# Optimization experiments

Measured on AMD Instinct MI355X. Metric: run time of the kernel, lower is better.

The kernel has to match this reference:

```python
import jax, jax.numpy as jnp
import numpy as np

NUM_GRAPHS = 128
EPS = 1e-5


def _instance_norm(x, seg, num_seg):
    # Per-graph instance norm over rows grouped by seg (PyG InstanceNorm, affine=False).
    ones = jnp.ones((x.shape[0], 1), x.dtype)
    cnt = jnp.maximum(jax.ops.segment_sum(ones, seg, num_segments=num_seg), 1.0)  # [G,1]
    mean = jax.ops.segment_sum(x, seg, num_segments=num_seg) / cnt               # [G,C]
    xc = x - mean[seg]
    var = jax.ops.segment_sum(xc * xc, seg, num_segments=num_seg) / cnt          # [G,C]
    return xc * jax.lax.rsqrt(var[seg] + EPS)


def setup_inputs() -> dict:
    key = jax.random.key(0)
    ks = jax.random.split(key, 8)
    N, E, H, G = 50000, 800000, 64, NUM_GRAPHS
    emb = jax.random.normal(ks[0], (N, H), dtype=jnp.float32)
    edge_index = jax.random.randint(ks[1], (2, E), 0, N, dtype=jnp.int64)
    batch = jnp.sort(jax.random.randint(ks[2], (N,), 0, G, dtype=jnp.int64))
    s1 = 1.0 / np.sqrt(2 * H)
    s2 = 1.0 / np.sqrt(4 * H)
    s3 = 1.0 / np.sqrt(H)
    return {
        "emb": emb,
        "edge_index": edge_index,
        "batch": batch,
        "W1": jax.random.normal(ks[3], (2 * H, 4 * H), dtype=jnp.float32) * s1,
        "b1": jnp.zeros((4 * H,), jnp.float32),
        "W2": jax.random.normal(ks[4], (4 * H, H), dtype=jnp.float32) * s2,
        "b2": jnp.zeros((H,), jnp.float32),
        "W3": jax.random.normal(ks[5], (H, 1), dtype=jnp.float32) * s3,
        "b3": jnp.zeros((1,), jnp.float32),
    }


def reference(emb, edge_index, batch, W1, b1, W2, b2, W3, b3):
    col, row = edge_index[0], edge_index[1]
    # Gather both endpoint embeddings and concat: [E, 2H]
    f12 = jnp.concatenate([emb[col], emb[row]], axis=-1)
    seg = batch[col]  # graph id per edge
    # MLP([2H, 4H, H, 1]): Linear -> InstanceNorm(batch) -> ReLU (dropout=identity in eval)
    h = jnp.maximum(_instance_norm(f12 @ W1 + b1, seg, NUM_GRAPHS), 0.0)
    h = jnp.maximum(_instance_norm(h @ W2 + b2, seg, NUM_GRAPHS), 0.0)
    att_log_logits = h @ W3 + b3  # [E, 1]
    return att_log_logits
```

## Files before the change

kernel.cpp:

```cpp
#include <hip/hip_runtime.h>
#include <hip/hip_bf16.h>
#include <stdint.h>

#define NG 128
#define EPSI 1e-5f

typedef __attribute__((ext_vector_type(8))) __bf16 bf16x8;
typedef __attribute__((ext_vector_type(4))) float f32x4;
typedef unsigned int u32x4 __attribute__((ext_vector_type(4)));

union ABFrag { bf16x8 v; unsigned short u[8]; uint4 q; };
union U8 { uint4 q; unsigned short u[8]; u32x4 e; };

__device__ __forceinline__ float b2f(unsigned short u){
  union { unsigned int i; float f; } v; v.i = ((unsigned int)u) << 16; return v.f;
}
__device__ __forceinline__ unsigned short f2b(float f){
  union { float f; unsigned int i; } v; v.f = f;
  unsigned int r = v.i + 0x7fffu + ((v.i >> 16) & 1u);
  return (unsigned short)(r >> 16);
}
__device__ __forceinline__ unsigned int pk2(float lo, float hi){
  unsigned int r;
  asm("v_cvt_pk_bf16_f32 %0, %1, %2" : "=v"(r) : "v"(lo), "v"(hi));
  return r;
}

__global__ void kprep(const float* __restrict__ emb, const float* __restrict__ W1,
                      const float* __restrict__ W2,
                      const int* __restrict__ ei,
                      unsigned short* __restrict__ embb, unsigned short* __restrict__ WcF,
                      unsigned short* __restrict__ W2F,
                      unsigned int* __restrict__ nodeh, int N, int E){
  int idx = blockIdx.x * 256 + threadIdx.x;
  int stride = gridDim.x * 256;
  int embCnt4 = N * 16;
  for (int i = idx; i < embCnt4; i += stride){
    float4 v = *(const float4*)(emb + (size_t)i * 4);
    ushort4 o; o.x = f2b(v.x); o.y = f2b(v.y); o.z = f2b(v.z); o.w = f2b(v.w);
    *(ushort4*)(embb + (size_t)i * 4) = o;
  }
  for (int i = idx; i < 32 * 2 * 64 * 8; i += stride){
    int j = i & 7, lane = (i >> 3) & 63, ks = (i >> 9) & 1, tn = i >> 10;
    int quad = lane >> 4, l15 = lane & 15;
    int k = ks * 32 + quad * 8 + j;
    int n = tn * 16 + l15;
    float wv = (n < 256) ? W1[k * 256 + n] : W1[(k + 64) * 256 + (n - 256)];
    WcF[i] = f2b(wv);
  }
  for (int i = idx; i < 4 * 8 * 64 * 8; i += stride){
    int j = i & 7, lane = (i >> 3) & 63, ks = (i >> 9) & 7, w = i >> 12;
    int quad = lane >> 4, l15 = lane & 15;
    W2F[i] = f2b(W2[(ks * 32 + quad * 8 + j) * 64 + w * 16 + l15]);
  }
  for (int e = idx; e < E; e += stride)
    atomicAdd(&nodeh[ei[e]], 1u);
}

__global__ void khist(const unsigned int* __restrict__ nodeh, const int* __restrict__ batch,
                      unsigned int* __restrict__ hist, int N){
  __shared__ unsigned int h[NG];
  for (int i = threadIdx.x; i < NG; i += 256) h[i] = 0;
  __syncthreads();
  int idx = blockIdx.x * 256 + threadIdx.x;
  for (int i = idx; i < N; i += gridDim.x * 256)
    atomicAdd(&h[batch[i]], nodeh[i]);
  __syncthreads();
  for (int i = threadIdx.x; i < NG; i += 256)
    if (h[i]) atomicAdd(&hist[i], h[i]);
}

__global__ void __launch_bounds__(256) kscan(const unsigned int* __restrict__ nodeh,
                      const unsigned int* __restrict__ hist,
                      const int* __restrict__ batch,
                      unsigned int* __restrict__ ncursor,
                      unsigned int* __restrict__ gmeta,
                      int* __restrict__ ecn, int* __restrict__ ern,
                      int* __restrict__ eorig, int* __restrict__ tilegid, int N){
  __shared__ unsigned int sh[3];
  __shared__ unsigned int wtot[4];
  int g = blockIdx.x;
  int t = threadIdx.x;
  unsigned int part = 0;
  for (int i = t; i < g; i += 256) part += (hist[i] + 31u) & ~31u;
  #pragma unroll
  for (int d = 1; d < 64; d <<= 1) part += __shfl_xor(part, d);
  if ((t & 63) == 0) wtot[t >> 6] = part;
  if (t == 64 || t == 65){
    int target = g + (t - 64);
    int lo = 0, hi = N;
    while (lo < hi){ int mid = (lo + hi) >> 1; if (batch[mid] < target) lo = mid + 1; else hi = mid; }
    sh[1 + (t - 64)] = lo;
  }
  __syncthreads();
  if (t == 0){
    unsigned int pb = wtot[0] + wtot[1] + wtot[2] + wtot[3];
    sh[0] = pb;
    gmeta[g] = pb;
    if (g == NG - 1) gmeta[NG] = pb + ((hist[g] + 31u) & ~31u);
  }
  __syncthreads();
  unsigned int run = sh[0];
  {
    unsigned int cnt = hist[g];
    unsigned int pe = (cnt + 31u) & ~31u;
    for (unsigned int i = cnt + t; i < pe; i += 256){
      ecn[run + i] = 0; ern[run + i] = 0; eorig[run + i] = -1;
    }
    unsigned int nt = pe >> 5, tb = run >> 5;
    for (unsigned int i = t; i < nt; i += 256) tilegid[tb + i] = g;
  }
  int lo = (int)sh[1], hi = (int)sh[2];
  int wid = t >> 6;
  for (int base = lo; base < hi; base += 256){
    int i = base + t;
    unsigned int v = (i < hi) ? nodeh[i] : 0u;
    unsigned int x = v;
    #pragma unroll
    for (int d = 1; d < 64; d <<= 1){
      unsigned int y = __shfl_up(x, d);
      if ((t & 63) >= d) x += y;
    }
    if ((t & 63) == 63) wtot[wid] = x;
    __syncthreads();
    unsigned int woff = 0;
    #pragma unroll
    for (int wb = 0; wb < 4; ++wb) if (wb < wid) woff += wtot[wb];
    if (i < hi) ncursor[i] = run + woff + x - v;
    run += wtot[0] + wtot[1] + wtot[2] + wtot[3];
    __syncthreads();
  }
}

__global__ void kscatter(const int* __restrict__ ei, int E,
                         unsigned int* __restrict__ ncursor,
                         int* __restrict__ ecn, int* __restrict__ ern,
                         int* __restrict__ eorig){
  int idx = blockIdx.x * 256 + threadIdx.x;
  for (int e = idx; e < E; e += gridDim.x * 256){
    int cn = ei[e], rn = ei[E + e];
    unsigned int p = atomicAdd(&ncursor[cn], 1u);
    ecn[p] = cn; ern[p] = rn; eorig[p] = e;
  }
}

__global__ void __launch_bounds__(256) kgemm1(const unsigned short* __restrict__ embb,
    const unsigned short* __restrict__ WcF, const float* __restrict__ b1,
    unsigned short* __restrict__ PQb, int Nn){
  int wave = threadIdx.x >> 6, lane = threadIdx.x & 63;
  int quad = lane >> 4, l15 = lane & 15;
  int tm = blockIdx.x * 4 + wave;
  int tmmax = (Nn + 15) >> 4;
  if (tm >= tmmax) return;
  int m = tm * 16 + l15; if (m >= Nn) m = Nn - 1;
  ABFrag a0, a1;
  a0.q = *(const uint4*)(embb + (size_t)m * 64 + quad * 8);
  a1.q = *(const uint4*)(embb + (size_t)m * 64 + 32 + quad * 8);
  int rowbase = tm * 16 + quad * 4;
  #pragma unroll 4
  for (int tn = 0; tn < 32; ++tn){
    ABFrag b0, b1f;
    b0.q  = *(const uint4*)(WcF + ((size_t)(tn * 2 + 0) * 64 + lane) * 8);
    b1f.q = *(const uint4*)(WcF + ((size_t)(tn * 2 + 1) * 64 + lane) * 8);
    f32x4 acc = {0.f, 0.f, 0.f, 0.f};
    acc = __builtin_amdgcn_mfma_f32_16x16x32_bf16(a0.v, b0.v, acc, 0, 0, 0);
    acc = __builtin_amdgcn_mfma_f32_16x16x32_bf16(a1.v, b1f.v, acc, 0, 0, 0);
    int col = tn * 16 + l15;
    float bias = (col < 256) ? b1[col] : 0.0f;
    #pragma unroll
    for (int r = 0; r < 4; ++r){
      int rowg = rowbase + r;
      if (rowg < Nn) PQb[(size_t)rowg * 512 + col] = f2b(acc[r] + bias);
    }
  }
}

__global__ void __launch_bounds__(256) kstats1(const unsigned short* __restrict__ PQb,
    const int* __restrict__ ern, const int* __restrict__ batch,
    const unsigned int* __restrict__ ncursor, const unsigned int* __restrict__ nodeh,
    float* __restrict__ sum1, float* __restrict__ sq1, int N){
  __shared__ float lsum[4][256];
  __shared__ float lsq[4][256];
  int tid = threadIdx.x;
  for (int i = tid; i < 4 * 256; i += 256){ ((float*)lsum)[i] = 0.f; ((float*)lsq)[i] = 0.f; }
  __syncthreads();
  int base = blockIdx.x * 32;
  int gfirst = batch[base];
  int wid = tid >> 6, lane = tid & 63;
  int c4 = lane * 4;
  float T1[4] = {0.f,0.f,0.f,0.f}, T2[4] = {0.f,0.f,0.f,0.f};
  int curg = -1;
  auto flushT = [&](){
    if (curg >= 0){
      unsigned slot = (unsigned)(curg - gfirst);
      if (slot < 4u){
        #pragma unroll
        for (int t = 0; t < 4; ++t){
          atomicAdd(&lsum[slot][c4 + t], T1[t]);
          atomicAdd(&lsq[slot][c4 + t], T2[t]);
        }
      } else {
        #pragma unroll
        for (int t = 0; t < 4; ++t){
          atomicAdd(&sum1[curg * 256 + c4 + t], T1[t]);
          atomicAdd(&sq1[curg * 256 + c4 + t], T2[t]);
        }
      }
      #pragma unroll
      for (int t = 0; t < 4; ++t){ T1[t] = 0.f; T2[t] = 0.f; }
    }
  };
  for (int i = 0; i < 8; ++i){
    int n = base + wid + i * 4;
    if (n >= N) break;
    int g = batch[n];
    unsigned int cnt = nodeh[n];
    if (g != curg){ flushT(); curg = g; }
    if (!cnt) continue;
    unsigned int start = ncursor[n] - cnt;
    ushort4 pv = *(const ushort4*)(PQb + (size_t)n * 512 + c4);
    float S1[4] = {0.f,0.f,0.f,0.f}, S2[4] = {0.f,0.f,0.f,0.f};
    for (unsigned int jb = 0; jb < cnt; jb += 64){
      int jn = (int)min(64u, cnt - jb);
      int rnv = (lane < jn) ? __builtin_nontemporal_load(&ern[start + jb + (unsigned)lane]) : 0;
      #pragma unroll 4
      for (int j = 0; j < jn; ++j){
        int rn = __shfl(rnv, j);
        ushort4 qv = *(const ushort4*)(PQb + (size_t)rn * 512 + 256 + c4);
        float q0 = b2f(qv.x), q1 = b2f(qv.y), q2 = b2f(qv.z), q3 = b2f(qv.w);
        S1[0] += q0; S2[0] = fmaf(q0, q0, S2[0]);
        S1[1] += q1; S2[1] = fmaf(q1, q1, S2[1]);
        S1[2] += q2; S2[2] = fmaf(q2, q2, S2[2]);
        S1[3] += q3; S2[3] = fmaf(q3, q3, S2[3]);
      }
    }
    float fc = (float)cnt;
    float p0 = b2f(pv.x), p1 = b2f(pv.y), p2 = b2f(pv.z), p3 = b2f(pv.w);
    T1[0] += fmaf(fc, p0, S1[0]);  T2[0] += fmaf(fmaf(fc, p0, 2.f * S1[0]), p0, S2[0]);
    T1[1] += fmaf(fc, p1, S1[1]);  T2[1] += fmaf(fmaf(fc, p1, 2.f * S1[1]), p1, S2[1]);
    T1[2] += fmaf(fc, p2, S1[2]);  T2[2] += fmaf(fmaf(fc, p2, 2.f * S1[2]), p2, S2[2]);
    T1[3] += fmaf(fc, p3, S1[3]);  T2[3] += fmaf(fmaf(fc, p3, 2.f * S1[3]), p3, S2[3]);
  }
  flushT();
  __syncthreads();
  for (int i = tid; i < 4 * 256; i += 256){
    int slot = i >> 8, ch = i & 255;
    float vs = lsum[slot][ch], vq = lsq[slot][ch];
    if (vs != 0.f || vq != 0.f){
      int g = gfirst + slot;
      atomicAdd(&sum1[g * 256 + ch], vs);
      atomicAdd(&sq1[g * 256 + ch], vq);
    }
  }
}

__global__ void kfin(const float* __restrict__ sum, const float* __restrict__ sq,
                     const unsigned int* __restrict__ hist,
                     float* __restrict__ meanA, float* __restrict__ rstdA, int C){
  int i = blockIdx.x * blockDim.x + threadIdx.x;
  if (i >= NG * C) return;
  int g = i / C;
  float cnt = fmaxf((float)hist[g], 1.0f);
  float m = sum[i] / cnt;
  float v = sq[i] / cnt - m * m;
  meanA[i] = m;
  rstdA[i] = rsqrtf(fmaxf(v, 0.f) + EPSI);
}

__global__ void __launch_bounds__(256) knorm1(unsigned short* __restrict__ PQb,
    const int* __restrict__ batch, const float* __restrict__ mean1,
    const float* __restrict__ rstd1, int N){
  int idx = blockIdx.x * 256 + threadIdx.x;
  if (idx >= N * 32) return;
  int n = idx >> 5, c8 = (idx & 31) * 8;
  int g = batch[n];
  unsigned short* pp = PQb + (size_t)n * 512 + c8;
  U8 pu; pu.q = *(const uint4*)pp;
  const float* mg = mean1 + g * 256 + c8;
  const float* rg = rstd1 + g * 256 + c8;
  float4 m0 = *(const float4*)mg, m1 = *(const float4*)(mg + 4);
  float4 r0 = *(const float4*)rg, r1 = *(const float4*)(rg + 4);
  U8 o;
  o.q.x = pk2((b2f(pu.u[0]) - m0.x) * r0.x, (b2f(pu.u[1]) - m0.y) * r0.y);
  o.q.y = pk2((b2f(pu.u[2]) - m0.z) * r0.z, (b2f(pu.u[3]) - m0.w) * r0.w);
  o.q.z = pk2((b2f(pu.u[4]) - m1.x) * r1.x, (b2f(pu.u[5]) - m1.y) * r1.y);
  o.q.w = pk2((b2f(pu.u[6]) - m1.z) * r1.z, (b2f(pu.u[7]) - m1.w) * r1.w);
  *(uint4*)pp = o.q;
}

__global__ void __launch_bounds__(256, 5) kmain(const unsigned short* __restrict__ PQb,
    const unsigned short* __restrict__ W2F,
    const int* __restrict__ ecn, const int* __restrict__ ern,
    const int* __restrict__ tilegid,
    const float* __restrict__ rstd1, const float* __restrict__ b2,
    const unsigned int* __restrict__ hist, const unsigned int* __restrict__ gmeta,
    unsigned short* __restrict__ y2b, float* __restrict__ sum2, float* __restrict__ sq2){
  __shared__ unsigned short Blds[4 * 8 * 64 * 8];
  {
    const uint4* src = (const uint4*)W2F;
    uint4* dst = (uint4*)Blds;
    for (int i = threadIdx.x; i < 2048; i += 256) dst[i] = src[i];
  }
  __syncthreads();
  int wave = threadIdx.x >> 6, lane = threadIdx.x & 63;
  int quad = lane >> 4, l15 = lane & 15;
  float b2v[4];
  #pragma unroll
  for (int cg = 0; cg < 4; ++cg) b2v[cg] = b2[cg * 16 + l15];
  int ntiles = (int)(gmeta[NG] >> 5);
  int nw = gridDim.x * 4;
  for (int t = blockIdx.x * 4 + wave; t < ntiles; t += nw){
    int p0 = t * 32;
    int g = __builtin_amdgcn_readfirstlane(tilegid[t]);
    int cn0 = __builtin_nontemporal_load(&ecn[p0 + l15]);
    int rn0 = __builtin_nontemporal_load(&ern[p0 + l15]);
    int cn1 = __builtin_nontemporal_load(&ecn[p0 + 16 + l15]);
    int rn1 = __builtin_nontemporal_load(&ern[p0 + 16 + l15]);
    const unsigned short* pp0 = PQb + (size_t)cn0 * 512 + quad * 8;
    const unsigned short* qq0 = PQb + (size_t)rn0 * 512 + 256 + quad * 8;
    const unsigned short* pp1 = PQb + (size_t)cn1 * 512 + quad * 8;
    const unsigned short* qq1 = PQb + (size_t)rn1 * 512 + 256 + quad * 8;
    const float* rr = rstd1 + g * 256 + quad * 8;
    f32x4 acc[8];
    #pragma unroll
    for (int i = 0; i < 8; ++i){ acc[i][0]=0.f; acc[i][1]=0.f; acc[i][2]=0.f; acc[i][3]=0.f; }
    #pragma unroll 2
    for (int ks = 0; ks < 8; ++ks){
      U8 pu0, qu0, pu1, qu1;
      pu0.q = *(const uint4*)(pp0 + ks * 32);
      qu0.q = *(const uint4*)(qq0 + ks * 32);
      pu1.q = *(const uint4*)(pp1 + ks * 32);
      qu1.q = *(const uint4*)(qq1 + ks * 32);
      float4 ra = *(const float4*)(rr + ks * 32);
      float4 rb = *(const float4*)(rr + ks * 32 + 4);
      ABFrag a0, a1;
      a0.q.x = pk2(fmaxf(0.f, b2f(pu0.u[0]) + b2f(qu0.u[0]) * ra.x),
                   fmaxf(0.f, b2f(pu0.u[1]) + b2f(qu0.u[1]) * ra.y));
      a0.q.y = pk2(fmaxf(0.f, b2f(pu0.u[2]) + b2f(qu0.u[2]) * ra.z),
                   fmaxf(0.f, b2f(pu0.u[3]) + b2f(qu0.u[3]) * ra.w));
      a0.q.z = pk2(fmaxf(0.f, b2f(pu0.u[4]) + b2f(qu0.u[4]) * rb.x),
                   fmaxf(0.f, b2f(pu0.u[5]) + b2f(qu0.u[5]) * rb.y));
      a0.q.w = pk2(fmaxf(0.f, b2f(pu0.u[6]) + b2f(qu0.u[6]) * rb.z),
                   fmaxf(0.f, b2f(pu0.u[7]) + b2f(qu0.u[7]) * rb.w));
      a1.q.x = pk2(fmaxf(0.f, b2f(pu1.u[0]) + b2f(qu1.u[0]) * ra.x),
                   fmaxf(0.f, b2f(pu1.u[1]) + b2f(qu1.u[1]) * ra.y));
      a1.q.y = pk2(fmaxf(0.f, b2f(pu1.u[2]) + b2f(qu1.u[2]) * ra.z),
                   fmaxf(0.f, b2f(pu1.u[3]) + b2f(qu1.u[3]) * ra.w));
      a1.q.z = pk2(fmaxf(0.f, b2f(pu1.u[4]) + b2f(qu1.u[4]) * rb.x),
                   fmaxf(0.f, b2f(pu1.u[5]) + b2f(qu1.u[5]) * rb.y));
      a1.q.w = pk2(fmaxf(0.f, b2f(pu1.u[6]) + b2f(qu1.u[6]) * rb.z),
                   fmaxf(0.f, b2f(pu1.u[7]) + b2f(qu1.u[7]) * rb.w));
      #pragma unroll
      for (int cg = 0; cg < 4; ++cg){
        ABFrag b;
        b.q = *(const uint4*)&Blds[((cg * 8 + ks) * 64 + lane) * 8];
        acc[cg]     = __builtin_amdgcn_mfma_f32_16x16x32_bf16(a0.v, b.v, acc[cg], 0, 0, 0);
        acc[4 + cg] = __builtin_amdgcn_mfma_f32_16x16x32_bf16(a1.v, b.v, acc[4 + cg], 0, 0, 0);
      }
    }
    #pragma unroll
    for (int sub = 0; sub < 2; ++sub)
      #pragma unroll
      for (int r = 0; r < 4; ++r){
        int el = sub * 16 + quad * 4 + r;
        size_t rowo = (size_t)(p0 + el) * 64 + l15;
        #pragma unroll
        for (int cg = 0; cg < 4; ++cg)
          y2b[rowo + cg * 16] = f2b(acc[sub * 4 + cg][r] + b2v[cg]);
      }
    int nl = (int)gmeta[g] + (int)hist[g] - p0;
    #pragma unroll
    for (int cg = 0; cg < 4; ++cg){
      float s = 0.f, qs = 0.f;
      #pragma unroll
      for (int sub = 0; sub < 2; ++sub)
        #pragma unroll
        for (int r = 0; r < 4; ++r){
          int el = sub * 16 + quad * 4 + r;
          if (el < nl){
            float y = acc[sub * 4 + cg][r] + b2v[cg];
            s += y; qs = fmaf(y, y, qs);
          }
        }
      s  += __shfl_xor(s, 16);  s  += __shfl_xor(s, 32);
      qs += __shfl_xor(qs, 16); qs += __shfl_xor(qs, 32);
      if (quad == 0){
        atomicAdd(&sum2[g * 64 + cg * 16 + l15], s);
        atomicAdd(&sq2[g * 64 + cg * 16 + l15], qs);
      }
    }
  }
}

__global__ void kfinal(const unsigned short* __restrict__ y2b,
                       const int* __restrict__ eorig, const int* __restrict__ tilegid,
                       const unsigned int* __restrict__ gmeta,
                       const float* __restrict__ mean2, const float* __restrict__ rstd2,
                       const float* __restrict__ W3, const float* __restrict__ b3,
                       float* __restrict__ out){
  int EP = (int)gmeta[NG];
  int sub = threadIdx.x & 7;
  int c8 = sub * 8;
  float w3r[8];
  #pragma unroll
  for (int t = 0; t < 8; ++t) w3r[t] = W3[c8 + t];
  float b3v = b3[0];
  int step = (gridDim.x * blockDim.x) >> 3;
  for (int i = (blockIdx.x * blockDim.x + threadIdx.x) >> 3; i < EP; i += step){
    int orig = __builtin_nontemporal_load(&eorig[i]);
    int gz = tilegid[i >> 5];
    U8 yv; yv.e = __builtin_nontemporal_load((const u32x4*)(y2b + (size_t)i * 64 + c8));
    const float* mg = mean2 + gz * 64 + c8;
    const float* rg = rstd2 + gz * 64 + c8;
    float4 m0 = *(const float4*)mg, m1 = *(const float4*)(mg + 4);
    float4 r0 = *(const float4*)rg, r1 = *(const float4*)(rg + 4);
    float a = 0.f;
    a += fmaxf(0.f, (b2f(yv.u[0]) - m0.x) * r0.x) * w3r[0];
    a += fmaxf(0.f, (b2f(yv.u[1]) - m0.y) * r0.y) * w3r[1];
    a += fmaxf(0.f, (b2f(yv.u[2]) - m0.z) * r0.z) * w3r[2];
    a += fmaxf(0.f, (b2f(yv.u[3]) - m0.w) * r0.w) * w3r[3];
    a += fmaxf(0.f, (b2f(yv.u[4]) - m1.x) * r1.x) * w3r[4];
    a += fmaxf(0.f, (b2f(yv.u[5]) - m1.y) * r1.y) * w3r[5];
    a += fmaxf(0.f, (b2f(yv.u[6]) - m1.z) * r1.z) * w3r[6];
    a += fmaxf(0.f, (b2f(yv.u[7]) - m1.w) * r1.w) * w3r[7];
    a += __shfl_xor(a, 1);
    a += __shfl_xor(a, 2);
    a += __shfl_xor(a, 4);
    if (sub == 0 && orig >= 0) out[orig] = a + b3v;
  }
}

extern "C" void kernel_launch(void* const* d_in, const int* in_sizes, int n_in,
                              void* d_out, int out_size, void* d_ws, size_t ws_size,
                              hipStream_t stream){
  const float* emb  = (const float*)d_in[0];
  const int*   ei   = (const int*)d_in[1];
  const int*   batch= (const int*)d_in[2];
  const float* W1   = (const float*)d_in[3];
  const float* b1   = (const float*)d_in[4];
  const float* W2   = (const float*)d_in[5];
  const float* b2   = (const float*)d_in[6];
  const float* W3   = (const float*)d_in[7];
  const float* b3   = (const float*)d_in[8];
  int N = in_sizes[0] / 64;
  int E = in_sizes[1] / 2;
  int EPMAX = E + NG * 32;
  float* out = (float*)d_out;

  char* w = (char*)d_ws;
  size_t off = 0;
  auto nxt = [&](size_t bytes) -> char* {
    char* p = w + off;
    off = (off + bytes + 255) & ~(size_t)255;
    return p;
  };
  unsigned short* embb = (unsigned short*)nxt((size_t)N * 64 * 2);
  unsigned short* WcF  = (unsigned short*)nxt(32 * 2 * 64 * 8 * 2);
  unsigned short* W2F  = (unsigned short*)nxt(4 * 8 * 64 * 8 * 2);
  unsigned short* PQb  = (unsigned short*)nxt((size_t)N * 512 * 2);
  unsigned short* y2b  = (unsigned short*)nxt((size_t)EPMAX * 64 * 2);
  int* ecn   = (int*)nxt((size_t)EPMAX * 4);
  int* ern   = (int*)nxt((size_t)EPMAX * 4);
  int* eorig = (int*)nxt((size_t)EPMAX * 4);
  int* tilegid = (int*)nxt((size_t)(EPMAX / 32 + 1) * 4);
  float* mean1 = (float*)nxt(NG * 256 * 4);
  float* rstd1 = (float*)nxt(NG * 256 * 4);
  float* mean2 = (float*)nxt(NG * 64 * 4);
  float* rstd2 = (float*)nxt(NG * 64 * 4);
  unsigned int* ncursor = (unsigned int*)nxt((size_t)N * 4);
  unsigned int* gmeta   = (unsigned int*)nxt((NG + 1) * 4);
  char* zbase = w + off;
  unsigned int* hist  = (unsigned int*)nxt(NG * 4);
  unsigned int* nodeh = (unsigned int*)nxt((size_t)N * 4);
  float* sum1 = (float*)nxt(NG * 256 * 4);
  float* sq1  = (float*)nxt(NG * 256 * 4);
  float* sum2 = (float*)nxt(NG * 64 * 4);
  float* sq2  = (float*)nxt(NG * 64 * 4);
  size_t zbytes = (size_t)((w + off) - zbase);
  hipMemsetAsync(zbase, 0, zbytes, stream);

  kprep<<<2048, 256, 0, stream>>>(emb, W1, W2, ei, embb, WcF, W2F, nodeh, N, E);
  khist<<<64, 256, 0, stream>>>(nodeh, batch, hist, N);
  kscan<<<NG, 256, 0, stream>>>(nodeh, hist, batch, ncursor, gmeta,
                                ecn, ern, eorig, tilegid, N);
  kscatter<<<2048, 256, 0, stream>>>(ei, E, ncursor, ecn, ern, eorig);
  {
    int tmmax = (N + 15) / 16;
    kgemm1<<<(tmmax + 3) / 4, 256, 0, stream>>>(embb, WcF, b1, PQb, N);
  }
  kstats1<<<(N + 31) / 32, 256, 0, stream>>>(PQb, ern, batch, ncursor, nodeh, sum1, sq1, N);
  kfin<<<(NG * 256 + 255) / 256, 256, 0, stream>>>(sum1, sq1, hist, mean1, rstd1, 256);
  knorm1<<<(N * 32 + 255) / 256, 256, 0, stream>>>(PQb, batch, mean1, rstd1, N);
  kmain<<<2048, 256, 0, stream>>>(PQb, W2F, ecn, ern, tilegid, rstd1, b2, hist, gmeta,
                                  y2b, sum2, sq2);
  kfin<<<(NG * 64 + 255) / 256, 256, 0, stream>>>(sum2, sq2, hist, mean2, rstd2, 64);
  kfinal<<<2048, 256, 0, stream>>>(y2b, eorig, tilegid, gmeta, mean2, rstd2, W3, b3, out);
}
```

Before: 454.3 us.

## Fuse emb bf16 conversion into GEMM1, write ecn in scan, swizzle kmain blocks

Drops the separate fp32-to-bf16 pass over the node embeddings; kgemm1 now loads fp32 rows and packs them to bf16 in registers. The column-node array is now filled in the scan kernel from the per-node prefix offsets, so the scatter kernel no longer writes it. kmain remaps block indices with an XCD-style swizzle so neighbouring tiles land on the same die, and kprep's grid size is halved. The scan's serial per-node fill loop may be unbalanced for high-degree nodes.

```diff
diff --git a/kernel.cpp b/kernel.cpp
--- a/kernel.cpp
+++ b/kernel.cpp
@@ -26,20 +26,12 @@
   return r;
 }
 
-__global__ void kprep(const float* __restrict__ emb, const float* __restrict__ W1,
-                      const float* __restrict__ W2,
+__global__ void kprep(const float* __restrict__ W1, const float* __restrict__ W2,
                       const int* __restrict__ ei,
-                      unsigned short* __restrict__ embb, unsigned short* __restrict__ WcF,
-                      unsigned short* __restrict__ W2F,
-                      unsigned int* __restrict__ nodeh, int N, int E){
+                      unsigned short* __restrict__ WcF, unsigned short* __restrict__ W2F,
+                      unsigned int* __restrict__ nodeh, int E){
   int idx = blockIdx.x * 256 + threadIdx.x;
   int stride = gridDim.x * 256;
-  int embCnt4 = N * 16;
-  for (int i = idx; i < embCnt4; i += stride){
-    float4 v = *(const float4*)(emb + (size_t)i * 4);
-    ushort4 o; o.x = f2b(v.x); o.y = f2b(v.y); o.z = f2b(v.z); o.w = f2b(v.w);
-    *(ushort4*)(embb + (size_t)i * 4) = o;
-  }
   for (int i = idx; i < 32 * 2 * 64 * 8; i += stride){
     int j = i & 7, lane = (i >> 3) & 63, ks = (i >> 9) & 1, tn = i >> 10;
     int quad = lane >> 4, l15 = lane & 15;
@@ -126,7 +118,11 @@
     unsigned int woff = 0;
     #pragma unroll
     for (int wb = 0; wb < 4; ++wb) if (wb < wid) woff += wtot[wb];
-    if (i < hi) ncursor[i] = run + woff + x - v;
+    if (i < hi){
+      unsigned int st = run + woff + x - v;
+      ncursor[i] = st;
+      for (unsigned int j = 0; j < v; ++j) ecn[st + j] = i;
+    }
     run += wtot[0] + wtot[1] + wtot[2] + wtot[3];
     __syncthreads();
   }
@@ -134,17 +130,16 @@
 
 __global__ void kscatter(const int* __restrict__ ei, int E,
                          unsigned int* __restrict__ ncursor,
-                         int* __restrict__ ecn, int* __restrict__ ern,
-                         int* __restrict__ eorig){
+                         int* __restrict__ ern, int* __restrict__ eorig){
   int idx = blockIdx.x * 256 + threadIdx.x;
   for (int e = idx; e < E; e += gridDim.x * 256){
     int cn = ei[e], rn = ei[E + e];
     unsigned int p = atomicAdd(&ncursor[cn], 1u);
-    ecn[p] = cn; ern[p] = rn; eorig[p] = e;
-  }
-}
-
-__global__ void __launch_bounds__(256) kgemm1(const unsigned short* __restrict__ embb,
+    ern[p] = rn; eorig[p] = e;
+  }
+}
+
+__global__ void __launch_bounds__(256) kgemm1(const float* __restrict__ emb,
     const unsigned short* __restrict__ WcF, const float* __restrict__ b1,
     unsigned short* __restrict__ PQb, int Nn){
   int wave = threadIdx.x >> 6, lane = threadIdx.x & 63;
@@ -153,9 +148,14 @@
   int tmmax = (Nn + 15) >> 4;
   if (tm >= tmmax) return;
   int m = tm * 16 + l15; if (m >= Nn) m = Nn - 1;
+  const float* er = emb + (size_t)m * 64 + quad * 8;
+  float4 f0 = *(const float4*)er,        f1 = *(const float4*)(er + 4);
+  float4 f2 = *(const float4*)(er + 32), f3 = *(const float4*)(er + 36);
   ABFrag a0, a1;
-  a0.q = *(const uint4*)(embb + (size_t)m * 64 + quad * 8);
-  a1.q = *(const uint4*)(embb + (size_t)m * 64 + 32 + quad * 8);
+  a0.q.x = pk2(f0.x, f0.y); a0.q.y = pk2(f0.z, f0.w);
+  a0.q.z = pk2(f1.x, f1.y); a0.q.w = pk2(f1.z, f1.w);
+  a1.q.x = pk2(f2.x, f2.y); a1.q.y = pk2(f2.z, f2.w);
+  a1.q.z = pk2(f3.x, f3.y); a1.q.w = pk2(f3.z, f3.w);
   int rowbase = tm * 16 + quad * 4;
   #pragma unroll 4
   for (int tn = 0; tn < 32; ++tn){
@@ -309,12 +309,15 @@
   for (int cg = 0; cg < 4; ++cg) b2v[cg] = b2[cg * 16 + l15];
   int ntiles = (int)(gmeta[NG] >> 5);
   int nw = gridDim.x * 4;
-  for (int t = blockIdx.x * 4 + wave; t < ntiles; t += nw){
+  int bid = blockIdx.x;
+  int nblk = gridDim.x;
+  int swz = ((nblk & 7) == 0) ? ((bid & 7) * (nblk >> 3) + (bid >> 3)) : bid;
+  for (int t = swz * 4 + wave; t < ntiles; t += nw){
     int p0 = t * 32;
     int g = __builtin_amdgcn_readfirstlane(tilegid[t]);
     int cn0 = __builtin_nontemporal_load(&ecn[p0 + l15]);
+    int cn1 = __builtin_nontemporal_load(&ecn[p0 + 16 + l15]);
     int rn0 = __builtin_nontemporal_load(&ern[p0 + l15]);
-    int cn1 = __builtin_nontemporal_load(&ecn[p0 + 16 + l15]);
     int rn1 = __builtin_nontemporal_load(&ern[p0 + 16 + l15]);
     const unsigned short* pp0 = PQb + (size_t)cn0 * 512 + quad * 8;
     const unsigned short* qq0 = PQb + (size_t)rn0 * 512 + 256 + quad * 8;
@@ -454,7 +457,6 @@
     off = (off + bytes + 255) & ~(size_t)255;
     return p;
   };
-  unsigned short* embb = (unsigned short*)nxt((size_t)N * 64 * 2);
   unsigned short* WcF  = (unsigned short*)nxt(32 * 2 * 64 * 8 * 2);
   unsigned short* W2F  = (unsigned short*)nxt(4 * 8 * 64 * 8 * 2);
   unsigned short* PQb  = (unsigned short*)nxt((size_t)N * 512 * 2);
@@ -479,14 +481,14 @@
   size_t zbytes = (size_t)((w + off) - zbase);
   hipMemsetAsync(zbase, 0, zbytes, stream);
 
-  kprep<<<2048, 256, 0, stream>>>(emb, W1, W2, ei, embb, WcF, W2F, nodeh, N, E);
+  kprep<<<1024, 256, 0, stream>>>(W1, W2, ei, WcF, W2F, nodeh, E);
   khist<<<64, 256, 0, stream>>>(nodeh, batch, hist, N);
   kscan<<<NG, 256, 0, stream>>>(nodeh, hist, batch, ncursor, gmeta,
                                 ecn, ern, eorig, tilegid, N);
-  kscatter<<<2048, 256, 0, stream>>>(ei, E, ncursor, ecn, ern, eorig);
+  kscatter<<<2048, 256, 0, stream>>>(ei, E, ncursor, ern, eorig);
   {
     int tmmax = (N + 15) / 16;
-    kgemm1<<<(tmmax + 3) / 4, 256, 0, stream>>>(embb, WcF, b1, PQb, N);
+    kgemm1<<<(tmmax + 3) / 4, 256, 0, stream>>>(emb, WcF, b1, PQb, N);
   }
   kstats1<<<(N + 31) / 32, 256, 0, stream>>>(PQb, ern, batch, ncursor, nodeh, sum1, sq1, N);
   kfin<<<(NG * 256 + 255) / 256, 256, 0, stream>>>(sum1, sq1, hist, mean1, rstd1, 256);
```

Measured after the change: 448.5 us. About the same (-1.3%).
